# Performance work log

Hardware: AMD Instinct MI355X
Metric: run time of the kernel (lower is better)

Reference implementation:

```python
import jax, jax.numpy as jnp
import numpy as np

B, H, W, C = 4, 256, 256, 16
NT = 9


def _rot2(a):
    c, s = np.cos(a), np.sin(a)
    return np.array([[c, -s], [s, c]])


def _aff(m2):
    p = np.eye(3)
    p[:2, :2] = m2
    return p


def _t(tx, ty):
    p = np.eye(3)
    p[0, 2] = tx
    p[1, 2] = ty
    return p


def _refl(direction):
    # reflection across line through origin spanned by `direction`
    v = np.asarray(direction, dtype=np.float64)
    m2 = 2.0 * np.outer(v, v) / np.dot(v, v) - np.eye(2)
    return _aff(m2)


def _get_transforms(t0, t1, t2):
    L = np.eye(3)
    L[:2, 0] = t1
    L[:2, 1] = t2
    L[:2, 2] = t0
    rot = lambda n: _aff(_rot2(2.0 * np.pi / n))
    e = np.eye(3)
    r2 = _t(.5, .5) @ rot(2) @ _t(-.5, -.5)
    r3 = _t(.5, .5) @ rot(3) @ _t(-.5, -.5)
    r4 = _t(.5, .5) @ rot(4) @ _t(-.5, -.5)
    r6 = _t(.5, .5) @ rot(6) @ _t(-.5, -.5)
    f_p = _t(0, .5) @ np.diag([1.0, -1.0, 1.0]) @ _t(0, -.5)
    f_c = np.array([[0.0, 1, 0], [1, 0, 0], [0, 0, 1]])
    f_l = _t(.5, .5) @ _refl(_rot2(5 * np.pi / 6) @ np.array([1.0, 0.0])) @ _t(-.5, -.5)
    f_s = _t(.5, .5) @ _refl(_rot2(np.pi / 3) @ np.array([1.0, 0.0])) @ _t(-.5, -.5)
    Ts = np.stack([e, r2, r3, r4, r6, f_p, f_c, f_l, f_s])
    Ts = L[None] @ Ts @ np.linalg.inv(L)[None]
    Ts = np.linalg.inv(Ts)
    Ts = Ts / Ts[:, 2:3, 2:3]  # normalize so last entry is 1
    return Ts.reshape(NT, 9)[:, :8].astype(np.float32)  # TF flat transform params


def setup_inputs() -> dict:
    key = jax.random.key(0)
    inputs = jax.random.normal(key, (B, H, W, C), dtype=jnp.float32)
    transforms = jnp.asarray(_get_transforms((0.0, 0.0), (float(H), 0.0), (0.0, float(W))))
    return {"inputs": inputs, "transforms": transforms}


def _warp_nearest(img, flat):
    # TF image_projective_transform_v2 semantics with NEAREST interpolation,
    # constant (zero) fill. flat maps OUTPUT (x,y) -> INPUT (x,y).
    b, h, w, c = img.shape
    yy, xx = jnp.meshgrid(jnp.arange(h, dtype=jnp.float32),
                          jnp.arange(w, dtype=jnp.float32), indexing="ij")
    a0, a1, a2, a3, a4, a5, a6, a7 = [flat[i] for i in range(8)]
    k = a6 * xx + a7 * yy + 1.0
    xi = jnp.round((a0 * xx + a1 * yy + a2) / k).astype(jnp.int32)
    yi = jnp.round((a3 * xx + a4 * yy + a5) / k).astype(jnp.int32)
    valid = (xi >= 0) & (xi < w) & (yi >= 0) & (yi < h)
    xi = jnp.clip(xi, 0, w - 1)
    yi = jnp.clip(yi, 0, h - 1)
    out = img[:, yi, xi, :]  # [b,h,w,c] gather
    return jnp.where(valid[None, :, :, None], out, 0.0)


def _forward(inputs, transforms):
    b, h, w, c = inputs.shape
    nt = transforms.shape[0]
    # warp the input by each of the nt group transforms: [nt,b,h,w,c]
    yw = jax.vmap(lambda m: _warp_nearest(inputs, m))(transforms)
    x = jnp.broadcast_to(inputs[None], yw.shape)
    x = jnp.transpose(x, (0, 1, 4, 2, 3))   # [nt,b,c,h,w]
    yw = jnp.transpose(yw, (0, 1, 4, 2, 3))
    # circular normalized cross-correlation via FFT, per channel image
    fx = jnp.fft.rfft2(x)
    fy = jnp.fft.rfft2(yw)
    corr = jnp.fft.irfft2(fx * jnp.conj(fy), s=(h, w))  # [nt,b,c,h,w]
    nx = jnp.linalg.norm(x.reshape(nt, b, c, -1), axis=-1)[..., None, None]
    ny = jnp.linalg.norm(yw.reshape(nt, b, c, -1), axis=-1)[..., None, None]
    corr = corr / (nx * ny + 1e-12)
    out = corr.mean(axis=2)                  # mean over channels -> [nt,b,h,w]
    return jnp.transpose(out, (1, 2, 3, 0))  # channels_last [b,h,w,nt]


def reference(inputs, transforms):
    return _forward(inputs, transforms)
```

## Files before the change

kernel.cpp:

```cpp
#include <hip/hip_runtime.h>
#include <hip/hip_fp16.h>

#define Bn  4
#define Hn  256
#define Wn  256
#define Cn  16
#define NTn 9
#define HWn (Hn*Wn)
#define KF  129
#define KGP 136
#define SRL 266
#define PI_F 3.14159265358979323846f

__device__ __forceinline__ int swz(int i) { return i ^ ((i >> 4) & 15); }

__device__ __forceinline__ void lds_fence() {
  __asm__ volatile("s_waitcnt lgkmcnt(0)" ::: "memory");
}

__device__ __forceinline__ float2 cmul(float2 a, float2 b) {
  float2 r = make_float2(a.x, a.x) * b;
  return r + make_float2(-a.y, a.y) * make_float2(b.y, b.x);
}

template<bool INV>
__device__ __forceinline__ void radix4(float2& x0, float2& x1, float2& x2, float2& x3) {
  float2 y0 = x0 + x2;
  float2 y1 = x0 - x2;
  float2 y2 = x1 + x3;
  float2 y3 = x1 - x3;
  float2 j3 = INV ? make_float2(-y3.y, y3.x) : make_float2(y3.y, -y3.x);
  x0 = y0 + y2;
  x2 = y0 - y2;
  x1 = y1 + j3;
  x3 = y1 - j3;
}

struct Tw { float2 a1,a2,a3,b1,b2,b3,c1,c2,c3; };

template<bool INV>
__device__ __forceinline__ Tw make_tw(int lane) {
  const float sgn = INV ? 2.0f * PI_F : -2.0f * PI_F;
  Tw t; float sw, cw;
  __sincosf(sgn * (float)lane / 256.0f, &sw, &cw);
  t.a1 = make_float2(cw, sw); t.a2 = cmul(t.a1, t.a1); t.a3 = cmul(t.a2, t.a1);
  __sincosf(sgn * (float)(lane & 15) / 64.0f, &sw, &cw);
  t.b1 = make_float2(cw, sw); t.b2 = cmul(t.b1, t.b1); t.b3 = cmul(t.b2, t.b1);
  __sincosf(sgn * (float)(lane & 3) / 16.0f, &sw, &cw);
  t.c1 = make_float2(cw, sw); t.c2 = cmul(t.c1, t.c1); t.c3 = cmul(t.c2, t.c1);
  return t;
}

template<bool INV, int NF>
__device__ __forceinline__ void fft256_n(float2 (*v)[4], float2 (*s)[SRL],
                                         int lane, const Tw& t) {
#pragma unroll
  for (int f = 0; f < NF; ++f) {
    radix4<INV>(v[f][0], v[f][1], v[f][2], v[f][3]);
    v[f][1] = cmul(v[f][1], t.a1); v[f][2] = cmul(v[f][2], t.a2); v[f][3] = cmul(v[f][3], t.a3);
#pragma unroll
    for (int a = 0; a < 4; ++a) s[f][swz(lane + (a << 6))] = v[f][a];
  }
  lds_fence();
  { int base = (lane >> 4) * 64 + (lane & 15);
#pragma unroll
    for (int f = 0; f < NF; ++f)
#pragma unroll
      for (int a = 0; a < 4; ++a) v[f][a] = s[f][swz(base + (a << 4))];
  }
  lds_fence();
#pragma unroll
  for (int f = 0; f < NF; ++f) {
    radix4<INV>(v[f][0], v[f][1], v[f][2], v[f][3]);
    v[f][1] = cmul(v[f][1], t.b1); v[f][2] = cmul(v[f][2], t.b2); v[f][3] = cmul(v[f][3], t.b3);
    int base = (lane >> 4) * 64 + (lane & 15);
#pragma unroll
    for (int a = 0; a < 4; ++a) s[f][swz(base + (a << 4))] = v[f][a];
  }
  lds_fence();
  { int base = (lane >> 4) * 64 + ((lane >> 2) & 3) * 16 + (lane & 3);
#pragma unroll
    for (int f = 0; f < NF; ++f)
#pragma unroll
      for (int a = 0; a < 4; ++a) v[f][a] = s[f][swz(base + (a << 2))];
  }
  lds_fence();
#pragma unroll
  for (int f = 0; f < NF; ++f) {
    radix4<INV>(v[f][0], v[f][1], v[f][2], v[f][3]);
    v[f][1] = cmul(v[f][1], t.c1); v[f][2] = cmul(v[f][2], t.c2); v[f][3] = cmul(v[f][3], t.c3);
    int base = (lane & ~3) * 4 + (lane & 3);
#pragma unroll
    for (int a = 0; a < 4; ++a) s[f][swz(base + (a << 2))] = v[f][a];
  }
  lds_fence();
  { int base = lane * 4;
#pragma unroll
    for (int f = 0; f < NF; ++f)
#pragma unroll
      for (int a = 0; a < 4; ++a) v[f][a] = s[f][swz(base + a)];
  }
  lds_fence();
  int dr = ((lane & 3) << 4) + (((lane >> 2) & 3) << 2) + (lane >> 4);
#pragma unroll
  for (int f = 0; f < NF; ++f) {
    radix4<INV>(v[f][0], v[f][1], v[f][2], v[f][3]);
#pragma unroll
    for (int a = 0; a < 4; ++a) s[f][swz(dr + (a << 6))] = v[f][a];
  }
  lds_fence();
}

__device__ __forceinline__ int warp_id2(float a0, float a2, float a3, float a5,
                                        float a6, float p1, float p4, float p7,
                                        bool affine, int col) {
#pragma clang fp contract(off)
  float x = (float)col;
  float xf = (a0 * x + p1) + a2;
  float yf = (a3 * x + p4) + a5;
  if (!affine) {
    float kk = (a6 * x + p7) + 1.0f;
    xf = xf / kk;
    yf = yf / kk;
  }
  float xr = rintf(xf), yr = rintf(yf);
  bool valid = (xr >= 0.f) && (xr < 256.f) && (yr >= 0.f) && (yr < 256.f);
  return valid ? ((int)yr * Wn + (int)xr) : -1;
}

__global__ __launch_bounds__(256) void k_yrow(const float* __restrict__ inp,
                                              const float* __restrict__ T,
                                              __half2* __restrict__ Yh,
                                              float* __restrict__ part) {
  __shared__ float2 sb[4][4][SRL];
  __shared__ float4 redw[4];
  int tid = threadIdx.x, w = tid >> 6, lane = tid & 63;
  Tw t = make_tw<false>(lane);
  int chunk = blockIdx.x & 15, cg = (blockIdx.x >> 4) & 3, tb = blockIdx.x >> 6;
  int b = tb & 3, tt = tb >> 2;
  int i0 = chunk << 4;
  const float4* ib = (const float4*)(inp + (size_t)b * HWn * Cn);
  float a0, a1, a2, a3, a4, a5, a6, a7;
  { const float* a = T + tt * 8;
    a0=a[0]; a1=a[1]; a2=a[2]; a3=a[3]; a4=a[4]; a5=a[5]; a6=a[6]; a7=a[7]; }
  const bool affine = (fabsf(a6) + fabsf(a7)) * 255.0f < 2.9e-8f;
  float4 nyacc = make_float4(0.f, 0.f, 0.f, 0.f);
  for (int h = 0; h < 2; ++h) {
    if (h) __syncthreads();
    int r0 = i0 + h * 8 + 2 * w;
    float yA = (float)r0, yB = (float)(r0 + 1);
    float p1A = a1 * yA, p4A = a4 * yA, p7A = a7 * yA;
    float p1B = a1 * yB, p4B = a4 * yB, p7B = a7 * yB;
    float4 g0[4], g1[4];
#pragma unroll
    for (int q = 0; q < 4; ++q) {
      int col = lane + (q << 6);
      int id0 = warp_id2(a0, a2, a3, a5, a6, p1A, p4A, p7A, affine, col);
      int id1 = warp_id2(a0, a2, a3, a5, a6, p1B, p4B, p7B, affine, col);
      g0[q] = (id0 >= 0) ? ib[(size_t)id0 * 4 + cg] : make_float4(0.f,0.f,0.f,0.f);
      g1[q] = (id1 >= 0) ? ib[(size_t)id1 * 4 + cg] : make_float4(0.f,0.f,0.f,0.f);
      nyacc += g0[q] * g0[q] + g1[q] * g1[q];
    }
    float2 v[4][4];
#pragma unroll
    for (int q = 0; q < 4; ++q) {
      v[0][q] = make_float2(g0[q].x, g1[q].x);
      v[1][q] = make_float2(g0[q].y, g1[q].y);
      v[2][q] = make_float2(g0[q].z, g1[q].z);
      v[3][q] = make_float2(g0[q].w, g1[q].w);
    }
    fft256_n<false, 4>(v, sb[w], lane, t);
    __syncthreads();
    int ii = tid & 7, kq = tid >> 3;
    int w2 = ii >> 1, odd = ii & 1;
#pragma unroll
    for (int p = 0; p < 5; ++p) {
      int k = p * 32 + kq;
      if (k <= 128) {
        int kc = (256 - k) & 255;
#pragma unroll
        for (int cc = 0; cc < 4; ++cc) {
          float2 Z  = sb[w2][cc][swz(k)];
          float2 Zc = sb[w2][cc][swz(kc)];
          float2 F = odd ? make_float2(0.5f * (Z.y + Zc.y), 0.5f * (Zc.x - Z.x))
                         : make_float2(0.5f * (Z.x + Zc.x), 0.5f * (Z.y - Zc.y));
          Yh[((size_t)(tb * Cn + cg * 4 + cc) * KF + k) * Hn + i0 + h * 8 + ii] =
              __float22half2_rn(F);
        }
      }
    }
  }
#pragma unroll
  for (int o = 32; o > 0; o >>= 1) {
    nyacc.x += __shfl_down(nyacc.x, o, 64);
    nyacc.y += __shfl_down(nyacc.y, o, 64);
    nyacc.z += __shfl_down(nyacc.z, o, 64);
    nyacc.w += __shfl_down(nyacc.w, o, 64);
  }
  if (lane == 0) redw[w] = nyacc;
  __syncthreads();
  if (tid == 0) {
    float4 s = make_float4(redw[0].x + redw[1].x + redw[2].x + redw[3].x,
                           redw[0].y + redw[1].y + redw[2].y + redw[3].y,
                           redw[0].z + redw[1].z + redw[2].z + redw[3].z,
                           redw[0].w + redw[1].w + redw[2].w + redw[3].w);
    part[((size_t)tb * Cn + cg * 4 + 0) * 16 + chunk] = s.x;
    part[((size_t)tb * Cn + cg * 4 + 1) * 16 + chunk] = s.y;
    part[((size_t)tb * Cn + cg * 4 + 2) * 16 + chunk] = s.z;
    part[((size_t)tb * Cn + cg * 4 + 3) * 16 + chunk] = s.w;
  }
}

__global__ __launch_bounds__(256) void k_colfft_fx(const __half2* __restrict__ Yh,
                                                   __half2* __restrict__ Fxh) {
  __shared__ float2 sb[4][4][SRL];
  int tid = threadIdx.x, w = tid >> 6, lane = tid & 63;
  Tw t = make_tw<false>(lane);
  int base_item = blockIdx.x * 16 + w * 4;
  float2 v[4][4];
#pragma unroll
  for (int f = 0; f < 4; ++f) {
    const __half2* Sp = Yh + (size_t)(base_item + f) * Hn;
#pragma unroll
    for (int q = 0; q < 4; ++q) v[f][q] = __half22float2(Sp[lane + (q << 6)]);
  }
  fft256_n<false, 4>(v, sb[w], lane, t);
#pragma unroll
  for (int f = 0; f < 4; ++f) {
    __half2* Op = Fxh + (size_t)(base_item + f) * Hn;
#pragma unroll
    for (int q = 0; q < 4; ++q) {
      int j = lane + (q << 6);
      Op[j] = __float22half2_rn(sb[w][f][swz(j)]);
    }
  }
}

__global__ __launch_bounds__(256) void k_ycol(const __half2* __restrict__ Yh,
                                              const __half2* __restrict__ Fxh,
                                              const float* __restrict__ part,
                                              float2* __restrict__ G) {
  __shared__ float2 sb[4][2][SRL];
  __shared__ float scs[16];
  int tid = threadIdx.x, w = tid >> 6, lane = tid & 63;
  int tb = blockIdx.x / 33, quart = blockIdx.x % 33;
  int b = tb & 3;
  if (tid < 16) {
    float sx = 0.f, sy = 0.f;
#pragma unroll
    for (int ch = 0; ch < 16; ++ch) {
      sx += part[((size_t)b  * Cn + tid) * 16 + ch];
      sy += part[((size_t)tb * Cn + tid) * 16 + ch];
    }
    scs[tid] = 1.0f / ((float)Cn * (sqrtf(sx) * sqrtf(sy) + 1e-12f));
  }
  __syncthreads();
  int k = quart * 4 + w;
  bool act = (k <= 128);
  if (act) {
    Tw tf = make_tw<false>(lane);
    float2 acc[4];
#pragma unroll
    for (int q = 0; q < 4; ++q) acc[q] = make_float2(0.f, 0.f);
    for (int c = 0; c < Cn; c += 2) {
      float2 v2[2][4];
#pragma unroll
      for (int e = 0; e < 2; ++e) {
        const __half2* Yp = Yh + ((size_t)(tb * Cn + c + e) * KF + k) * Hn;
#pragma unroll
        for (int q = 0; q < 4; ++q) v2[e][q] = __half22float2(Yp[lane + (q << 6)]);
      }
      fft256_n<false, 2>(v2, sb[w], lane, tf);
#pragma unroll
      for (int e = 0; e < 2; ++e) {
        float sc = scs[c + e];
        const __half2* Fxp = Fxh + ((size_t)(b * Cn + c + e) * KF + k) * Hn;
#pragma unroll
        for (int q = 0; q < 4; ++q) {
          int rr = lane + (q << 6);
          float2 fy = sb[w][e][swz(rr)];
          float2 fx = __half22float2(Fxp[rr]);
          float2 pr = make_float2(fy.x, fy.x) * fx
                    + make_float2(fy.y, fy.y) * make_float2(fx.y, -fx.x);
          acc[q] += make_float2(sc, sc) * pr;
        }
      }
    }
    Tw ti = make_tw<true>(lane);
    fft256_n<true, 1>(reinterpret_cast<float2(*)[4]>(acc), sb[w], lane, ti);
  }
  __syncthreads();
  int kk = tid & 3, jj0 = tid >> 2;
  if (quart * 4 + kk <= 128) {
    float2* Gp = G + ((size_t)tb * Hn) * KGP + quart * 4 + kk;
#pragma unroll
    for (int p = 0; p < 4; ++p) {
      int j = jj0 + (p << 6);
      Gp[(size_t)j * KGP] = sb[kk][0][swz(j)];
    }
  }
}

__global__ __launch_bounds__(320) void k_irow(const float2* __restrict__ G,
                                              float* __restrict__ out) {
  __shared__ float2 tile[5][2][132];
  __shared__ float2 sb[5][SRL];
  __shared__ float rowbuf[Wn * NTn];
  int tid = threadIdx.x, w = tid >> 6, lane = tid & 63;
  Tw ti = make_tw<true>(lane);
  int b = blockIdx.x >> 8, i = blockIdx.x & 255;
  const float scale = 1.0f / ((float)Hn * (float)Wn);
  int t1 = 2 * w, t2 = t1 + 1;
  {
    const float2* Gp1 = G + ((size_t)(t1 * Bn + b) * Hn + i) * KGP;
    for (int k = lane; k < KF; k += 64) tile[w][0][k] = Gp1[k];
    if (t2 < NTn) {
      const float2* Gp2 = G + ((size_t)(t2 * Bn + b) * Hn + i) * KGP;
      for (int k = lane; k < KF; k += 64) tile[w][1][k] = Gp2[k];
    }
  }
  lds_fence();
  float2 v[1][4];
#pragma unroll
  for (int q = 0; q < 4; ++q) {
    int k = lane + (q << 6);
    float2 a, bb;
    if (k <= 128) a = tile[w][0][k];
    else { float2 z = tile[w][0][256 - k]; a = make_float2(z.x, -z.y); }
    if (t2 < NTn) {
      if (k <= 128) bb = tile[w][1][k];
      else { float2 z = tile[w][1][256 - k]; bb = make_float2(z.x, -z.y); }
    } else bb = make_float2(0.f, 0.f);
    v[0][q] = a + make_float2(-bb.y, bb.x);
  }
  fft256_n<true, 1>(v, reinterpret_cast<float2(*)[SRL]>(sb[w]), lane, ti);
#pragma unroll
  for (int q = 0; q < 4; ++q) {
    int j = lane + (q << 6);
    float2 r = sb[w][swz(j)];
    rowbuf[j * NTn + t1] = r.x * scale;
    if (t2 < NTn) rowbuf[j * NTn + t2] = r.y * scale;
  }
  __syncthreads();
  float* ob = out + ((size_t)(b * Hn + i) * Wn) * NTn;
  for (int f = tid; f < Wn * NTn; f += 320) ob[f] = rowbuf[f];
}

extern "C" void kernel_launch(void* const* d_in, const int* in_sizes, int n_in,
                              void* d_out, int out_size, void* d_ws, size_t ws_size,
                              hipStream_t stream) {
  const float* inp = (const float*)d_in[0];
  const float* T   = (const float*)d_in[1];
  float* out = (float*)d_out;
  char* ws = (char*)d_ws;

  size_t off = 0;
  float*   part = (float*)(ws + off);  off += (size_t)NTn * Bn * Cn * 16 * sizeof(float);
  __half2* Fxh = (__half2*)(ws + off); off += (size_t)Bn * Cn * KF * Hn * sizeof(__half2);
  float2*  G   = (float2*)(ws + off);  off += (size_t)NTn * Bn * Hn * KGP * sizeof(float2);
  __half2* Yh  = (__half2*)(ws + off); off += (size_t)NTn * Bn * Cn * KF * Hn * sizeof(__half2);
  (void)off; (void)ws_size; (void)in_sizes; (void)n_in; (void)out_size;

  k_yrow<<<NTn * Bn * 64, 256, 0, stream>>>(inp, T, Yh, part);
  k_colfft_fx<<<Bn * Cn * KF / 4 / 4, 256, 0, stream>>>(Yh, Fxh);
  k_ycol<<<NTn * Bn * 33, 256, 0, stream>>>(Yh, Fxh, part, G);
  k_irow<<<Bn * Hn, 320, 0, stream>>>(G, out);
}
```

Baseline: 178.7 us.

## Prefetch second-half gathers during first-half spectrum store in k_yrow

Splits the two-iteration row-FFT loop so that the gathered inputs for the second 8-row half are loaded into registers before the first half's spectra are written out. Global gather latency can then overlap with the half-precision stores. Also adds a launch-bounds occupancy hint and remaps block indices so that consecutive blocks spread across batch images. The prefetch raises register pressure, which the occupancy hint may cap and so cause spills.

```diff
diff --git a/kernel.cpp b/kernel.cpp
--- a/kernel.cpp
+++ b/kernel.cpp
@@ -128,16 +128,19 @@
   return valid ? ((int)yr * Wn + (int)xr) : -1;
 }
 
-__global__ __launch_bounds__(256) void k_yrow(const float* __restrict__ inp,
-                                              const float* __restrict__ T,
-                                              __half2* __restrict__ Yh,
-                                              float* __restrict__ part) {
+__global__ __launch_bounds__(256, 4) void k_yrow(const float* __restrict__ inp,
+                                                 const float* __restrict__ T,
+                                                 __half2* __restrict__ Yh,
+                                                 float* __restrict__ part) {
   __shared__ float2 sb[4][4][SRL];
   __shared__ float4 redw[4];
   int tid = threadIdx.x, w = tid >> 6, lane = tid & 63;
   Tw t = make_tw<false>(lane);
-  int chunk = blockIdx.x & 15, cg = (blockIdx.x >> 4) & 3, tb = blockIdx.x >> 6;
-  int b = tb & 3, tt = tb >> 2;
+  int slot = blockIdx.x & 7, idx = blockIdx.x >> 3;
+  int b = slot >> 1;
+  int rem = (slot & 1) * 288 + idx;
+  int tt = rem >> 6, cg = (rem >> 4) & 3, chunk = rem & 15;
+  int tb = tt * 4 + b;
   int i0 = chunk << 4;
   const float4* ib = (const float4*)(inp + (size_t)b * HWn * Cn);
   float a0, a1, a2, a3, a4, a5, a6, a7;
@@ -145,32 +148,8 @@
     a0=a[0]; a1=a[1]; a2=a[2]; a3=a[3]; a4=a[4]; a5=a[5]; a6=a[6]; a7=a[7]; }
   const bool affine = (fabsf(a6) + fabsf(a7)) * 255.0f < 2.9e-8f;
   float4 nyacc = make_float4(0.f, 0.f, 0.f, 0.f);
-  for (int h = 0; h < 2; ++h) {
-    if (h) __syncthreads();
-    int r0 = i0 + h * 8 + 2 * w;
-    float yA = (float)r0, yB = (float)(r0 + 1);
-    float p1A = a1 * yA, p4A = a4 * yA, p7A = a7 * yA;
-    float p1B = a1 * yB, p4B = a4 * yB, p7B = a7 * yB;
-    float4 g0[4], g1[4];
-#pragma unroll
-    for (int q = 0; q < 4; ++q) {
-      int col = lane + (q << 6);
-      int id0 = warp_id2(a0, a2, a3, a5, a6, p1A, p4A, p7A, affine, col);
-      int id1 = warp_id2(a0, a2, a3, a5, a6, p1B, p4B, p7B, affine, col);
-      g0[q] = (id0 >= 0) ? ib[(size_t)id0 * 4 + cg] : make_float4(0.f,0.f,0.f,0.f);
-      g1[q] = (id1 >= 0) ? ib[(size_t)id1 * 4 + cg] : make_float4(0.f,0.f,0.f,0.f);
-      nyacc += g0[q] * g0[q] + g1[q] * g1[q];
-    }
-    float2 v[4][4];
-#pragma unroll
-    for (int q = 0; q < 4; ++q) {
-      v[0][q] = make_float2(g0[q].x, g1[q].x);
-      v[1][q] = make_float2(g0[q].y, g1[q].y);
-      v[2][q] = make_float2(g0[q].z, g1[q].z);
-      v[3][q] = make_float2(g0[q].w, g1[q].w);
-    }
-    fft256_n<false, 4>(v, sb[w], lane, t);
-    __syncthreads();
+
+  auto store_half = [&](int h) {
     int ii = tid & 7, kq = tid >> 3;
     int w2 = ii >> 1, odd = ii & 1;
 #pragma unroll
@@ -189,7 +168,71 @@
         }
       }
     }
-  }
+  };
+
+  {
+    int r0 = i0 + 2 * w;
+    float yA = (float)r0, yB = (float)(r0 + 1);
+    float p1A = a1 * yA, p4A = a4 * yA, p7A = a7 * yA;
+    float p1B = a1 * yB, p4B = a4 * yB, p7B = a7 * yB;
+    float4 g0[4], g1[4];
+#pragma unroll
+    for (int q = 0; q < 4; ++q) {
+      int col = lane + (q << 6);
+      int id0 = warp_id2(a0, a2, a3, a5, a6, p1A, p4A, p7A, affine, col);
+      int id1 = warp_id2(a0, a2, a3, a5, a6, p1B, p4B, p7B, affine, col);
+      g0[q] = (id0 >= 0) ? ib[(size_t)id0 * 4 + cg] : make_float4(0.f,0.f,0.f,0.f);
+      g1[q] = (id1 >= 0) ? ib[(size_t)id1 * 4 + cg] : make_float4(0.f,0.f,0.f,0.f);
+      nyacc += g0[q] * g0[q] + g1[q] * g1[q];
+    }
+    float2 v[4][4];
+#pragma unroll
+    for (int q = 0; q < 4; ++q) {
+      v[0][q] = make_float2(g0[q].x, g1[q].x);
+      v[1][q] = make_float2(g0[q].y, g1[q].y);
+      v[2][q] = make_float2(g0[q].z, g1[q].z);
+      v[3][q] = make_float2(g0[q].w, g1[q].w);
+    }
+    fft256_n<false, 4>(v, sb[w], lane, t);
+  }
+  __syncthreads();
+
+  float4 G0[4], G1[4];
+  {
+    int r1 = i0 + 8 + 2 * w;
+    float yA = (float)r1, yB = (float)(r1 + 1);
+    float p1A = a1 * yA, p4A = a4 * yA, p7A = a7 * yA;
+    float p1B = a1 * yB, p4B = a4 * yB, p7B = a7 * yB;
+#pragma unroll
+    for (int q = 0; q < 4; ++q) {
+      int col = lane + (q << 6);
+      int id0 = warp_id2(a0, a2, a3, a5, a6, p1A, p4A, p7A, affine, col);
+      int id1 = warp_id2(a0, a2, a3, a5, a6, p1B, p4B, p7B, affine, col);
+      G0[q] = (id0 >= 0) ? ib[(size_t)id0 * 4 + cg] : make_float4(0.f,0.f,0.f,0.f);
+      G1[q] = (id1 >= 0) ? ib[(size_t)id1 * 4 + cg] : make_float4(0.f,0.f,0.f,0.f);
+    }
+  }
+
+  store_half(0);
+  __syncthreads();
+
+  {
+#pragma unroll
+    for (int q = 0; q < 4; ++q)
+      nyacc += G0[q] * G0[q] + G1[q] * G1[q];
+    float2 v[4][4];
+#pragma unroll
+    for (int q = 0; q < 4; ++q) {
+      v[0][q] = make_float2(G0[q].x, G1[q].x);
+      v[1][q] = make_float2(G0[q].y, G1[q].y);
+      v[2][q] = make_float2(G0[q].z, G1[q].z);
+      v[3][q] = make_float2(G0[q].w, G1[q].w);
+    }
+    fft256_n<false, 4>(v, sb[w], lane, t);
+  }
+  __syncthreads();
+  store_half(1);
+
 #pragma unroll
   for (int o = 32; o > 0; o >>= 1) {
     nyacc.x += __shfl_down(nyacc.x, o, 64);
```

Result: slower. 206.6 us (+15.6%).
